# Kernel optimization log

Measured on AMD Instinct MI355X. Metric: run time of the kernel, lower is better.

The kernel has to match this reference:

```python
import jax, jax.numpy as jnp
import numpy as np

HEAD_DIM = 128
MROPE_SECTION = (16, 24, 24)  # sums to HEAD_DIM // 2
ROPE_THETA = 1000000.0
NEG_INF = -2.3819763e38


def _mrope_cos_sin(positions, theta, mrope_section, head_dim):
    # positions: [3, B, T] int; returns cos, sin of shape [B, T, head_dim]
    half = head_dim // 2
    inv_freq = 1.0 / (theta ** (jnp.arange(half, dtype=jnp.float32) * 2.0 / head_dim))
    angles = positions.astype(jnp.float32)[..., None] * inv_freq  # [3, B, T, half]
    sec = np.cumsum([0] + list(mrope_section))
    # pick temporal/height/width channel per frequency band
    angles_sel = jnp.concatenate(
        [angles[j, ..., sec[j]:sec[j + 1]] for j in range(3)], axis=-1
    )  # [B, T, half]
    cos = jnp.cos(angles_sel)
    sin = jnp.sin(angles_sel)
    cos = jnp.concatenate([cos, cos], axis=-1)  # [B, T, head_dim]
    sin = jnp.concatenate([sin, sin], axis=-1)
    return cos, sin


def _apply_rope(x, cos, sin):
    # x: [B, T, n, H]; cos/sin: [B, T, H]
    half = x.shape[-1] // 2
    x1, x2 = x[..., :half], x[..., half:]
    rot = jnp.concatenate([-x2, x1], axis=-1)
    return x * cos[:, :, None, :] + rot * sin[:, :, None, :]


def setup_inputs() -> dict:
    key = jax.random.key(0)
    ks = jax.random.split(key, 8)
    B, T, D = 2, 512, 3584
    N, K, H = 28, 4, 128
    S_CACHE = 3584
    S = S_CACHE + T
    x = jax.random.normal(ks[0], (B, T, D), dtype=jnp.float32)
    wq = jax.random.normal(ks[1], (N, D, H), dtype=jnp.float32) * (D ** -0.5)
    wk = jax.random.normal(ks[2], (K, D, H), dtype=jnp.float32) * (D ** -0.5)
    wv = jax.random.normal(ks[3], (K, D, H), dtype=jnp.float32) * (D ** -0.5)
    wo = jax.random.normal(ks[4], (N, H, D), dtype=jnp.float32) * ((N * H) ** -0.5)
    cache_k = jax.random.normal(ks[5], (B, S_CACHE, K, H), dtype=jnp.float32)
    cache_v = jax.random.normal(ks[6], (B, S_CACHE, K, H), dtype=jnp.float32)
    # positions continue after the cache; all 3 mrope channels identical (text)
    pos1d = S_CACHE + jnp.arange(T, dtype=jnp.int32)
    positions = jnp.broadcast_to(pos1d[None, None, :], (3, B, T))
    # mask: full visibility into cache, causal within the new block
    causal = jnp.tril(jnp.ones((T, T), dtype=bool))
    attn_mask = jnp.concatenate(
        [jnp.ones((T, S_CACHE), dtype=bool), causal], axis=-1
    )[None, None].repeat(B, axis=0)  # [B, 1, T, S]
    return {"x": x, "positions": positions, "attn_mask": attn_mask,
            "cache_k": cache_k, "cache_v": cache_v,
            "wq": wq, "wk": wk, "wv": wv, "wo": wo}


def reference(x, positions, attn_mask, cache_k, cache_v, wq, wk, wv, wo):
    N, K, H = wq.shape[0], wk.shape[0], wq.shape[2]
    G = N // K
    q = jnp.einsum('BTD,NDH->BTNH', x, wq)
    k = jnp.einsum('BSD,KDH->BSKH', x, wk)
    v = jnp.einsum('BSD,KDH->BSKH', x, wv)
    cos, sin = _mrope_cos_sin(positions, ROPE_THETA, MROPE_SECTION, H)
    q = _apply_rope(q, cos, sin)
    k = _apply_rope(k, cos, sin)
    q = q * (H ** -0.5)
    k = jnp.concatenate([cache_k, k], axis=1)  # [B, S, K, H]
    v = jnp.concatenate([cache_v, v], axis=1)
    cached_k, cached_v = k, v
    B, T = q.shape[0], q.shape[1]
    qg = q.reshape(B, T, K, G, H)
    # GQA: broadcast each kv head over its G query-head group (same math as repeat_kv)
    logits = jnp.einsum('BTKGH,BSKH->BKGTS', qg, k,
                        preferred_element_type=jnp.float32)
    masked = jnp.where(attn_mask[:, :, None, :, :], logits, NEG_INF)
    probs = jax.nn.softmax(masked, axis=-1).astype(x.dtype)
    encoded = jnp.einsum('BKGTS,BSKH->BTKGH', probs, v).reshape(B, T, N, H)
    out = jnp.einsum('BTNH,NHD->BTD', encoded, wo)
    return out, cached_k, cached_v
```

## Files before the change

kernel.cpp:

```cpp
#include <hip/hip_runtime.h>
#include <cstdint>
#include <cstddef>
#include <cmath>

typedef __bf16 bf16;
typedef __bf16 bf16x8 __attribute__((ext_vector_type(8)));
typedef float f32x4 __attribute__((ext_vector_type(4)));

__device__ __forceinline__ f32x4 mfma_bf16(bf16x8 a, bf16x8 b, f32x4 c) {
  return __builtin_amdgcn_mfma_f32_16x16x32_bf16(a, b, c, 0, 0, 0);
}

union U8 { bf16 h[8]; uint4 u; };
__device__ __forceinline__ uint4 cvt8(float4 a, float4 b) {
  U8 t;
  t.h[0] = (bf16)a.x; t.h[1] = (bf16)a.y; t.h[2] = (bf16)a.z; t.h[3] = (bf16)a.w;
  t.h[4] = (bf16)b.x; t.h[5] = (bf16)b.y; t.h[6] = (bf16)b.z; t.h[7] = (bf16)b.w;
  return t.u;
}

__device__ __forceinline__ bf16x8 ones8() {
  union { uint4 u; bf16x8 h; } t;
  t.u = make_uint4(0x3F803F80u, 0x3F803F80u, 0x3F803F80u, 0x3F803F80u);
  return t.h;
}

__device__ __forceinline__ void gload_lds16(const bf16* g, bf16* l) {
  __builtin_amdgcn_global_load_lds((const __attribute__((address_space(1))) void*)g,
                                   (__attribute__((address_space(3))) void*)l, 16, 0, 0);
}

__global__ __launch_bounds__(256) void prep(const float* __restrict__ ck,
                                            const float* __restrict__ cv,
                                            float* __restrict__ cko,
                                            float* __restrict__ cvo,
                                            bf16* __restrict__ kb_t,
                                            const float* __restrict__ x,
                                            bf16* __restrict__ xb,
                                            const int* __restrict__ pos,
                                            float* __restrict__ cosb,
                                            float* __restrict__ sinb) {
  size_t idx = (size_t)blockIdx.x * 256 + threadIdx.x;
  size_t e = idx * 8;
  size_t b = e / 1835008u, re = e % 1835008u;
  size_t de = b * 2097152u + re;
  float4 k0 = *(const float4*)(ck + e), k1 = *(const float4*)(ck + e + 4);
  float4 v0 = *(const float4*)(cv + e), v1 = *(const float4*)(cv + e + 4);
  *(float4*)(cko + de) = k0; *(float4*)(cko + de + 4) = k1;
  *(float4*)(cvo + de) = v0; *(float4*)(cvo + de + 4) = v1;
  {
    int s = (int)(re >> 9);
    int rem = (int)(re & 511);
    int khh = rem >> 7, h0 = rem & 127;
    size_t dk = ((size_t)(b * 4 + khh) * 128 + (s >> 5)) * 4096 + (size_t)(s & 31) * 128 + h0;
    *(uint4*)(kb_t + dk) = cvt8(k0, k1);
  }
  *(uint4*)(xb + e) = cvt8(*(const float4*)(x + e), *(const float4*)(x + e + 4));
  if (idx < 65536) {
    int m = (int)(idx >> 6), i = (int)(idx & 63);
    int j = (i < 16) ? 0 : ((i < 40) ? 1 : 2);
    float p = (float)pos[j * 1024 + m];
    float invf = (float)exp((double)i * -0.21586735246819178);
    float a = p * invf;
    cosb[m * 64 + i] = cosf(a);
    sinb[m * 64 + i] = sinf(a);
  }
}

__global__ __launch_bounds__(256) void transpose_f2b(const float* __restrict__ src,
                                                     bf16* __restrict__ dst,
                                                     int R, int C) {
  const size_t ms = (size_t)R * C;
  const float* s = src + (size_t)blockIdx.z * ms;
  bf16* d = dst + (size_t)blockIdx.z * ms;
  const int c0 = blockIdx.x * 64, r0 = blockIdx.y * 64;
  __shared__ bf16 tile[64 * 72];
  const int tid = threadIdx.x;
#pragma unroll
  for (int it = 0; it < 2; ++it) {
    int slot = tid + it * 256;
    int r = slot >> 3, c8 = slot & 7;
    const float* p = s + (size_t)(r0 + r) * C + c0 + c8 * 8;
    *(uint4*)(tile + r * 72 + c8 * 8) = cvt8(*(const float4*)p, *(const float4*)(p + 4));
  }
  __syncthreads();
#pragma unroll
  for (int it = 0; it < 2; ++it) {
    int slot = tid + it * 256;
    int c = slot >> 3, r8 = slot & 7;
    U8 tmp;
#pragma unroll
    for (int jj = 0; jj < 8; ++jj) tmp.h[jj] = tile[(r8 * 8 + jj) * 72 + c];
    *(uint4*)(d + (size_t)(c0 + c) * R + r0 + r8 * 8) = tmp.u;
  }
}

__global__ __launch_bounds__(256) void transpose_qkv(const float* __restrict__ wq,
                                                     const float* __restrict__ wk,
                                                     const float* __restrict__ wv,
                                                     bf16* __restrict__ dst) {
  const size_t ms = (size_t)3584 * 128;
  const int z = blockIdx.z;
  const float* s = (z < 28) ? wq + (size_t)z * ms
                 : (z < 32) ? wk + (size_t)(z - 28) * ms
                            : wv + (size_t)(z - 32) * ms;
  bf16* d = dst + (size_t)z * ms;
  const int c0 = blockIdx.x * 64, r0 = blockIdx.y * 64;
  __shared__ bf16 tile[64 * 72];
  const int tid = threadIdx.x;
#pragma unroll
  for (int it = 0; it < 2; ++it) {
    int slot = tid + it * 256;
    int r = slot >> 3, c8 = slot & 7;
    const float* p = s + (size_t)(r0 + r) * 128 + c0 + c8 * 8;
    *(uint4*)(tile + r * 72 + c8 * 8) = cvt8(*(const float4*)p, *(const float4*)(p + 4));
  }
  __syncthreads();
#pragma unroll
  for (int it = 0; it < 2; ++it) {
    int slot = tid + it * 256;
    int c = slot >> 3, r8 = slot & 7;
    U8 tmp;
#pragma unroll
    for (int jj = 0; jj < 8; ++jj) tmp.h[jj] = tile[(r8 * 8 + jj) * 72 + c];
    *(uint4*)(d + (size_t)(c0 + c) * 3584 + r0 + r8 * 8) = tmp.u;
  }
}

__global__ __launch_bounds__(256) void transpose_v(const float* __restrict__ cvo,
                                                   bf16* __restrict__ vt_t) {
  const int b = blockIdx.z >> 2, kh = blockIdx.z & 3;
  const int s0 = blockIdx.x * 64, h0 = blockIdx.y * 64;
  __shared__ bf16 tile[64 * 72];
  const int tid = threadIdx.x;
#pragma unroll
  for (int it = 0; it < 2; ++it) {
    int slot = tid + it * 256;
    int r = slot >> 3, c8 = slot & 7;
    const float* p = cvo + (size_t)((b * 4096 + s0 + r) * 4 + kh) * 128 + h0 + c8 * 8;
    *(uint4*)(tile + r * 72 + c8 * 8) = cvt8(*(const float4*)p, *(const float4*)(p + 4));
  }
  __syncthreads();
#pragma unroll
  for (int it = 0; it < 2; ++it) {
    int slot = tid + it * 256;
    int c = slot >> 3, r8 = slot & 7;
    U8 tmp;
#pragma unroll
    for (int jj = 0; jj < 8; ++jj) tmp.h[jj] = tile[(r8 * 8 + jj) * 72 + c];
    int s = s0 + r8 * 8;
    *(uint4*)(vt_t + ((size_t)((b * 4 + kh) * 128 + (s >> 5))) * 4096 +
              (size_t)(h0 + c) * 32 + (s & 31)) = tmp.u;
  }
}

template <int MODE>
__global__ __launch_bounds__(256) void gemm128(
    const bf16* __restrict__ A, const bf16* __restrict__ Bt,
    bf16* __restrict__ q_ws, float* __restrict__ cko, bf16* __restrict__ kb_t,
    float* __restrict__ cvo, const float* __restrict__ cosb,
    const float* __restrict__ sinb, float* __restrict__ outp) {
  const int cb = blockIdx.x;
  const int m0 = blockIdx.y * 128;
  const int tid = threadIdx.x;
  const int wave = tid >> 6, lane = tid & 63;
  const int c16 = lane & 15, q4 = lane >> 4;
  __shared__ bf16 lA[2][128 * 64];
  __shared__ bf16 lB[2][128 * 64];

  int offA[2][2], offB[8][2];
#pragma unroll
  for (int i = 0; i < 2; ++i) {
    int rA = wave * 32 + i * 16 + c16;
#pragma unroll
    for (int kk = 0; kk < 2; ++kk) offA[i][kk] = rA * 64 + (kk * 4 + q4) * 8;
  }
#pragma unroll
  for (int j = 0; j < 8; ++j) {
    int rB = j * 16 + c16;
#pragma unroll
    for (int kk = 0; kk < 2; ++kk) offB[j][kk] = rB * 64 + (kk * 4 + q4) * 8;
  }

  f32x4 acc[2][8];
#pragma unroll
  for (int i = 0; i < 2; ++i)
#pragma unroll
    for (int j = 0; j < 8; ++j) acc[i][j] = (f32x4){0.f, 0.f, 0.f, 0.f};

#pragma unroll
  for (int it = 0; it < 4; ++it) {
    int slot = tid + it * 256;
    gload_lds16(A + (size_t)(m0 + (slot >> 3)) * 3584 + (slot & 7) * 8, &lA[0][slot * 8]);
    gload_lds16(Bt + (size_t)(cb * 128 + (slot >> 3)) * 3584 + (slot & 7) * 8, &lB[0][slot * 8]);
  }
  __syncthreads();

  for (int k0 = 0; k0 < 3584; k0 += 64) {
    const int cur = (k0 >> 6) & 1;
    if (k0 + 64 < 3584) {
#pragma unroll
      for (int it = 0; it < 4; ++it) {
        int slot = tid + it * 256;
        gload_lds16(A + (size_t)(m0 + (slot >> 3)) * 3584 + k0 + 64 + (slot & 7) * 8,
                    &lA[cur ^ 1][slot * 8]);
        gload_lds16(Bt + (size_t)(cb * 128 + (slot >> 3)) * 3584 + k0 + 64 + (slot & 7) * 8,
                    &lB[cur ^ 1][slot * 8]);
      }
    }
#pragma unroll
    for (int kk = 0; kk < 2; ++kk) {
      bf16x8 av0 = *(const bf16x8*)(&lA[cur][offA[0][kk]]);
      bf16x8 av1 = *(const bf16x8*)(&lA[cur][offA[1][kk]]);
#pragma unroll
      for (int j = 0; j < 8; ++j) {
        bf16x8 bv = *(const bf16x8*)(&lB[cur][offB[j][kk]]);
        acc[0][j] = mfma_bf16(av0, bv, acc[0][j]);
        acc[1][j] = mfma_bf16(av1, bv, acc[1][j]);
      }
    }
    __syncthreads();
  }

  if (MODE == 1) {
#pragma unroll
    for (int i = 0; i < 2; ++i) {
      int mb = m0 + wave * 32 + i * 16 + q4 * 4;
#pragma unroll
      for (int r = 0; r < 4; ++r) {
        size_t rowoff = (size_t)(mb + r) * 3584 + cb * 128;
#pragma unroll
        for (int j = 0; j < 8; ++j) outp[rowoff + j * 16 + c16] = acc[i][j][r];
      }
    }
    return;
  }

  const int head = cb;
#pragma unroll
  for (int i = 0; i < 2; ++i) {
    int mb = m0 + wave * 32 + i * 16 + q4 * 4;
#pragma unroll
    for (int r = 0; r < 4; ++r) {
      int m = mb + r;
      int bb = m >> 9, tt = m & 511;
      if (head < 32) {
        const float* cp = cosb + m * 64;
        const float* sp = sinb + m * 64;
#pragma unroll
        for (int j = 0; j < 4; ++j) {
          int h = j * 16 + c16;
          float c = cp[h], s = sp[h];
          float v1 = acc[i][j][r], v2 = acc[i][j + 4][r];
          float o1 = v1 * c - v2 * s;
          float o2 = v2 * c + v1 * s;
          if (head < 28) {
            const float QS = 0.08838834764831845f;
            size_t base = ((size_t)m * 28 + head) * 128;
            q_ws[base + h] = (bf16)(o1 * QS);
            q_ws[base + h + 64] = (bf16)(o2 * QS);
          } else {
            int sg = 3584 + tt;
            size_t base = ((size_t)((bb * 4096 + sg) * 4 + (head - 28))) * 128;
            cko[base + h] = o1;
            cko[base + h + 64] = o2;
            size_t bt = ((size_t)(bb * 4 + (head - 28)) * 128 + (sg >> 5)) * 4096 +
                        (size_t)(sg & 31) * 128;
            kb_t[bt + h] = (bf16)o1;
            kb_t[bt + h + 64] = (bf16)o2;
          }
        }
      } else {
        size_t base = ((size_t)((bb * 4096 + 3584 + tt) * 4 + (head - 32))) * 128;
#pragma unroll
        for (int j = 0; j < 8; ++j) cvo[base + j * 16 + c16] = acc[i][j][r];
      }
    }
  }
}

__global__ __launch_bounds__(512) void attn_kernel(const bf16* __restrict__ q_ws,
                                                   const bf16* __restrict__ kb_t,
                                                   const bf16* __restrict__ vt_t,
                                                   bf16* __restrict__ p0,
                                                   bf16* __restrict__ p1,
                                                   bf16* __restrict__ p2,
                                                   float* __restrict__ lp) {
  const int combo = blockIdx.x & 7;
  const int b = combo >> 2, kh = combo & 3;
  const int rest = blockIdx.x >> 3;
  const int third = rest % 3;
  const int t0 = (rest / 3) * 16;
  const int tid = threadIdx.x;
  const int wave = tid >> 6, lane = tid & 63;
  const int c16 = lane & 15, q4 = lane >> 4;

  __shared__ bf16 Kc[2][4096];
  __shared__ bf16 Vc[2][4096];
  __shared__ bf16 Ps[8][16 * 40];

  const int kr = tid >> 4, ksl = tid & 15;
  const int ksrc = kr * 128 + ((ksl ^ (kr & 7)) * 8);
  const int vh = tid >> 2, vsl = tid & 3;
  const int vsrc = vh * 32 + ((vsl ^ ((vh >> 1) & 3)) * 8);
  const bf16* kcb = kb_t + (size_t)((b * 4 + kh) * 128) * 4096;
  const bf16* vcb = vt_t + (size_t)((b * 4 + kh) * 128) * 4096;

  int koff[2][4];
#pragma unroll
  for (int kk = 0; kk < 4; ++kk) {
    int ph = ((q4 * 16 + kk * 64) ^ ((c16 & 7) << 4)) >> 1;
    koff[0][kk] = c16 * 128 + ph;
    koff[1][kk] = (c16 + 16) * 128 + ph;
  }
  int voff[8];
#pragma unroll
  for (int jo = 0; jo < 8; ++jo)
    voff[jo] = (jo * 16 + c16) * 32 + ((q4 ^ ((c16 >> 1) & 3)) * 8);

  const int n = kh * 7 + wave;
  bf16x8 aQ[4];
  if (wave < 7) {
    const bf16* qbase = q_ws + ((size_t)((b * 512 + t0 + c16) * 28 + n)) * 128 + q4 * 8;
#pragma unroll
    for (int kk = 0; kk < 4; ++kk) aQ[kk] = *(const bf16x8*)(qbase + kk * 32);
  }

  f32x4 accO[8];
  f32x4 accL = (f32x4){0.f, 0.f, 0.f, 0.f};
#pragma unroll
  for (int j = 0; j < 8; ++j) accO[j] = (f32x4){0.f, 0.f, 0.f, 0.f};
  const bf16x8 vone = ones8();
  bf16* pw = Ps[wave];

  const int nch = (3631 + t0) >> 5;
  const int lo = (nch * third) / 3, hi = (nch * (third + 1)) / 3;

  gload_lds16(kcb + (size_t)lo * 4096 + ksrc, &Kc[0][tid * 8]);
  gload_lds16(vcb + (size_t)lo * 4096 + vsrc, &Vc[0][tid * 8]);
  __syncthreads();

  for (int c = lo; c < hi; ++c) {
    const int cur = (c - lo) & 1;
    if (c + 1 < hi) {
      gload_lds16(kcb + (size_t)(c + 1) * 4096 + ksrc, &Kc[cur ^ 1][tid * 8]);
      gload_lds16(vcb + (size_t)(c + 1) * 4096 + vsrc, &Vc[cur ^ 1][tid * 8]);
    }
    if (wave < 7) {
      const int s0 = c * 32;
      const bf16* kc = Kc[cur];
      const bf16* vc = Vc[cur];
      f32x4 accS0 = (f32x4){0.f, 0.f, 0.f, 0.f};
      f32x4 accS1 = (f32x4){0.f, 0.f, 0.f, 0.f};
#pragma unroll
      for (int kk = 0; kk < 4; ++kk) {
        bf16x8 bK0 = *(const bf16x8*)(&kc[koff[0][kk]]);
        bf16x8 bK1 = *(const bf16x8*)(&kc[koff[1][kk]]);
        accS0 = mfma_bf16(aQ[kk], bK0, accS0);
        accS1 = mfma_bf16(aQ[kk], bK1, accS1);
      }

      if (s0 + 31 > 3584 + t0) {
#pragma unroll
        for (int r = 0; r < 4; ++r) {
          int lim = 3584 + t0 + q4 * 4 + r - s0;
          float x0 = (c16 <= lim) ? __expf(accS0[r]) : 0.f;
          float x1 = (16 + c16 <= lim) ? __expf(accS1[r]) : 0.f;
          int prow = (q4 * 4 + r) * 40;
          pw[prow + c16] = (bf16)x0;
          pw[prow + 16 + c16] = (bf16)x1;
        }
      } else {
#pragma unroll
        for (int r = 0; r < 4; ++r) {
          int prow = (q4 * 4 + r) * 40;
          pw[prow + c16] = (bf16)__expf(accS0[r]);
          pw[prow + 16 + c16] = (bf16)__expf(accS1[r]);
        }
      }

      bf16x8 aP = *(const bf16x8*)(pw + c16 * 40 + q4 * 8);
      accL = mfma_bf16(aP, vone, accL);
#pragma unroll
      for (int jo = 0; jo < 8; ++jo) {
        bf16x8 bV = *(const bf16x8*)(&vc[voff[jo]]);
        accO[jo] = mfma_bf16(aP, bV, accO[jo]);
      }
    }
    __syncthreads();
  }

  if (wave < 7) {
    bf16* pb = (third == 0) ? p0 : (third == 1) ? p1 : p2;
#pragma unroll
    for (int r = 0; r < 4; ++r) {
      int tg = t0 + q4 * 4 + r;
      size_t row = (size_t)(b * 512 + tg) * 28 + n;
      size_t base = row * 128;
#pragma unroll
      for (int jo = 0; jo < 8; ++jo)
        pb[base + jo * 16 + c16] = (bf16)accO[jo][r];
      if (c16 == 0) lp[third * 57344 + row] = accL[r];
    }
  }
}

__global__ __launch_bounds__(256) void attn_merge(const bf16* __restrict__ p0,
                                                  const bf16* __restrict__ p1,
                                                  const bf16* __restrict__ p2,
                                                  const float* __restrict__ lp,
                                                  bf16* __restrict__ enc) {
  size_t idx = (size_t)blockIdx.x * 256 + threadIdx.x;
  size_t e = idx * 8;
  size_t row = e >> 7;
  float l = lp[row] + lp[57344 + row] + lp[114688 + row];
  float inv = 1.0f / l;
  bf16x8 a = *(const bf16x8*)(p0 + e);
  bf16x8 b8 = *(const bf16x8*)(p1 + e);
  bf16x8 c8 = *(const bf16x8*)(p2 + e);
  U8 o;
#pragma unroll
  for (int j = 0; j < 8; ++j)
    o.h[j] = (bf16)(((float)a[j] + (float)b8[j] + (float)c8[j]) * inv);
  *(uint4*)(enc + e) = o.u;
}

extern "C" void kernel_launch(void* const* d_in, const int* in_sizes, int n_in,
                              void* d_out, int out_size, void* d_ws, size_t ws_size,
                              hipStream_t stream) {
  const float* x = (const float*)d_in[0];
  const int* pos = (const int*)d_in[1];
  const float* ck = (const float*)d_in[3];
  const float* cv = (const float*)d_in[4];
  const float* wq = (const float*)d_in[5];
  const float* wk = (const float*)d_in[6];
  const float* wv = (const float*)d_in[7];
  const float* wo = (const float*)d_in[8];

  float* out = (float*)d_out;
  float* cko = out + 3670016;
  float* cvo = cko + 4194304;

  bf16* wqkvT = (bf16*)d_ws;
  bf16* woT = wqkvT;
  bf16* p2 = wqkvT + 12845056;
  bf16* xb = wqkvT + 16515072;
  bf16* q_ws = xb + 3670016;
  bf16* encw = q_ws + 3670016;
  bf16* kb_t = encw + 3670016;
  bf16* vt_t = kb_t + 4194304;
  float* cosb = (float*)(vt_t + 4194304);
  float* sinb = cosb + 65536;
  float* lp = out;
  if (ws_size < 72351744ull) return;

  prep<<<1792, 256, 0, stream>>>(ck, cv, cko, cvo, kb_t, x, xb, pos, cosb, sinb);
  transpose_qkv<<<dim3(2, 56, 36), 256, 0, stream>>>(wq, wk, wv, wqkvT);
  gemm128<0><<<dim3(36, 8), 256, 0, stream>>>(xb, wqkvT, q_ws, cko, kb_t, cvo, cosb, sinb, nullptr);
  transpose_f2b<<<dim3(56, 56, 1), 256, 0, stream>>>(wo, woT, 3584, 3584);
  transpose_v<<<dim3(64, 2, 8), 256, 0, stream>>>(cvo, vt_t);
  attn_kernel<<<768, 512, 0, stream>>>(q_ws, kb_t, vt_t, encw, xb, p2, lp);
  attn_merge<<<1792, 256, 0, stream>>>(encw, xb, p2, lp, encw);
  gemm128<1><<<dim3(28, 8), 256, 0, stream>>>(encw, woT, nullptr, nullptr, nullptr, nullptr,
                                              nullptr, nullptr, out);
}
```

Baseline: 471.9 us.

## Use 512-thread GEMM blocks and register-shuffle P in attention instead of LDS

The GEMM kernels now launch 512 threads per 128x128 tile, with each of 8 waves owning 16 rows instead of 32. This halves accumulators per thread and raises wave count per CU, which may help latency hiding. The attention kernel swaps the MFMA operand order so S is produced transposed, then packs exp(S) to bf16 in registers and redistributes it with shfl_xor and v_permlane32_swap. This removes the per-chunk LDS round trip for P and its scratch buffer, at the cost of extra cross-lane instructions and reliance on the correct lane mapping.

```diff
diff --git a/kernel.cpp b/kernel.cpp
--- a/kernel.cpp
+++ b/kernel.cpp
@@ -28,6 +28,12 @@
 __device__ __forceinline__ void gload_lds16(const bf16* g, bf16* l) {
   __builtin_amdgcn_global_load_lds((const __attribute__((address_space(1))) void*)g,
                                    (__attribute__((address_space(3))) void*)l, 16, 0, 0);
+}
+
+__device__ __forceinline__ unsigned cvt_pk_bf16(float lo, float hi) {
+  unsigned r;
+  asm("v_cvt_pk_bf16_f32 %0, %1, %2" : "=v"(r) : "v"(lo), "v"(hi));
+  return r;
 }
 
 __global__ __launch_bounds__(256) void prep(const float* __restrict__ ck,
@@ -155,7 +161,7 @@
 }
 
 template <int MODE>
-__global__ __launch_bounds__(256) void gemm128(
+__global__ __launch_bounds__(512) void gemm128(
     const bf16* __restrict__ A, const bf16* __restrict__ Bt,
     bf16* __restrict__ q_ws, float* __restrict__ cko, bf16* __restrict__ kb_t,
     float* __restrict__ cvo, const float* __restrict__ cosb,
@@ -168,13 +174,9 @@
   __shared__ bf16 lA[2][128 * 64];
   __shared__ bf16 lB[2][128 * 64];
 
-  int offA[2][2], offB[8][2];
-#pragma unroll
-  for (int i = 0; i < 2; ++i) {
-    int rA = wave * 32 + i * 16 + c16;
-#pragma unroll
-    for (int kk = 0; kk < 2; ++kk) offA[i][kk] = rA * 64 + (kk * 4 + q4) * 8;
-  }
+  int offA[2], offB[8][2];
+#pragma unroll
+  for (int kk = 0; kk < 2; ++kk) offA[kk] = (wave * 16 + c16) * 64 + (kk * 4 + q4) * 8;
 #pragma unroll
   for (int j = 0; j < 8; ++j) {
     int rB = j * 16 + c16;
@@ -182,15 +184,13 @@
     for (int kk = 0; kk < 2; ++kk) offB[j][kk] = rB * 64 + (kk * 4 + q4) * 8;
   }
 
-  f32x4 acc[2][8];
-#pragma unroll
-  for (int i = 0; i < 2; ++i)
-#pragma unroll
-    for (int j = 0; j < 8; ++j) acc[i][j] = (f32x4){0.f, 0.f, 0.f, 0.f};
-
-#pragma unroll
-  for (int it = 0; it < 4; ++it) {
-    int slot = tid + it * 256;
+  f32x4 acc[8];
+#pragma unroll
+  for (int j = 0; j < 8; ++j) acc[j] = (f32x4){0.f, 0.f, 0.f, 0.f};
+
+#pragma unroll
+  for (int it = 0; it < 2; ++it) {
+    int slot = tid + it * 512;
     gload_lds16(A + (size_t)(m0 + (slot >> 3)) * 3584 + (slot & 7) * 8, &lA[0][slot * 8]);
     gload_lds16(Bt + (size_t)(cb * 128 + (slot >> 3)) * 3584 + (slot & 7) * 8, &lB[0][slot * 8]);
   }
@@ -200,8 +200,8 @@
     const int cur = (k0 >> 6) & 1;
     if (k0 + 64 < 3584) {
 #pragma unroll
-      for (int it = 0; it < 4; ++it) {
-        int slot = tid + it * 256;
+      for (int it = 0; it < 2; ++it) {
+        int slot = tid + it * 512;
         gload_lds16(A + (size_t)(m0 + (slot >> 3)) * 3584 + k0 + 64 + (slot & 7) * 8,
                     &lA[cur ^ 1][slot * 8]);
         gload_lds16(Bt + (size_t)(cb * 128 + (slot >> 3)) * 3584 + k0 + 64 + (slot & 7) * 8,
@@ -210,71 +210,63 @@
     }
 #pragma unroll
     for (int kk = 0; kk < 2; ++kk) {
-      bf16x8 av0 = *(const bf16x8*)(&lA[cur][offA[0][kk]]);
-      bf16x8 av1 = *(const bf16x8*)(&lA[cur][offA[1][kk]]);
+      bf16x8 av = *(const bf16x8*)(&lA[cur][offA[kk]]);
 #pragma unroll
       for (int j = 0; j < 8; ++j) {
         bf16x8 bv = *(const bf16x8*)(&lB[cur][offB[j][kk]]);
-        acc[0][j] = mfma_bf16(av0, bv, acc[0][j]);
-        acc[1][j] = mfma_bf16(av1, bv, acc[1][j]);
+        acc[j] = mfma_bf16(av, bv, acc[j]);
       }
     }
     __syncthreads();
   }
 
   if (MODE == 1) {
-#pragma unroll
-    for (int i = 0; i < 2; ++i) {
-      int mb = m0 + wave * 32 + i * 16 + q4 * 4;
-#pragma unroll
-      for (int r = 0; r < 4; ++r) {
-        size_t rowoff = (size_t)(mb + r) * 3584 + cb * 128;
-#pragma unroll
-        for (int j = 0; j < 8; ++j) outp[rowoff + j * 16 + c16] = acc[i][j][r];
-      }
+    int mb = m0 + wave * 16 + q4 * 4;
+#pragma unroll
+    for (int r = 0; r < 4; ++r) {
+      size_t rowoff = (size_t)(mb + r) * 3584 + cb * 128;
+#pragma unroll
+      for (int j = 0; j < 8; ++j) outp[rowoff + j * 16 + c16] = acc[j][r];
     }
     return;
   }
 
   const int head = cb;
-#pragma unroll
-  for (int i = 0; i < 2; ++i) {
-    int mb = m0 + wave * 32 + i * 16 + q4 * 4;
-#pragma unroll
-    for (int r = 0; r < 4; ++r) {
-      int m = mb + r;
-      int bb = m >> 9, tt = m & 511;
-      if (head < 32) {
-        const float* cp = cosb + m * 64;
-        const float* sp = sinb + m * 64;
-#pragma unroll
-        for (int j = 0; j < 4; ++j) {
-          int h = j * 16 + c16;
-          float c = cp[h], s = sp[h];
-          float v1 = acc[i][j][r], v2 = acc[i][j + 4][r];
-          float o1 = v1 * c - v2 * s;
-          float o2 = v2 * c + v1 * s;
-          if (head < 28) {
-            const float QS = 0.08838834764831845f;
-            size_t base = ((size_t)m * 28 + head) * 128;
-            q_ws[base + h] = (bf16)(o1 * QS);
-            q_ws[base + h + 64] = (bf16)(o2 * QS);
-          } else {
-            int sg = 3584 + tt;
-            size_t base = ((size_t)((bb * 4096 + sg) * 4 + (head - 28))) * 128;
-            cko[base + h] = o1;
-            cko[base + h + 64] = o2;
-            size_t bt = ((size_t)(bb * 4 + (head - 28)) * 128 + (sg >> 5)) * 4096 +
-                        (size_t)(sg & 31) * 128;
-            kb_t[bt + h] = (bf16)o1;
-            kb_t[bt + h + 64] = (bf16)o2;
-          }
+  int mb = m0 + wave * 16 + q4 * 4;
+#pragma unroll
+  for (int r = 0; r < 4; ++r) {
+    int m = mb + r;
+    int bb = m >> 9, tt = m & 511;
+    if (head < 32) {
+      const float* cp = cosb + m * 64;
+      const float* sp = sinb + m * 64;
+#pragma unroll
+      for (int j = 0; j < 4; ++j) {
+        int h = j * 16 + c16;
+        float c = cp[h], s = sp[h];
+        float v1 = acc[j][r], v2 = acc[j + 4][r];
+        float o1 = v1 * c - v2 * s;
+        float o2 = v2 * c + v1 * s;
+        if (head < 28) {
+          const float QS = 0.08838834764831845f;
+          size_t base = ((size_t)m * 28 + head) * 128;
+          q_ws[base + h] = (bf16)(o1 * QS);
+          q_ws[base + h + 64] = (bf16)(o2 * QS);
+        } else {
+          int sg = 3584 + tt;
+          size_t base = ((size_t)((bb * 4096 + sg) * 4 + (head - 28))) * 128;
+          cko[base + h] = o1;
+          cko[base + h + 64] = o2;
+          size_t bt = ((size_t)(bb * 4 + (head - 28)) * 128 + (sg >> 5)) * 4096 +
+                      (size_t)(sg & 31) * 128;
+          kb_t[bt + h] = (bf16)o1;
+          kb_t[bt + h + 64] = (bf16)o2;
         }
-      } else {
-        size_t base = ((size_t)((bb * 4096 + 3584 + tt) * 4 + (head - 32))) * 128;
-#pragma unroll
-        for (int j = 0; j < 8; ++j) cvo[base + j * 16 + c16] = acc[i][j][r];
-      }
+      }
+    } else {
+      size_t base = ((size_t)((bb * 4096 + 3584 + tt) * 4 + (head - 32))) * 128;
+#pragma unroll
+      for (int j = 0; j < 8; ++j) cvo[base + j * 16 + c16] = acc[j][r];
     }
   }
 }
@@ -297,7 +289,6 @@
 
   __shared__ bf16 Kc[2][4096];
   __shared__ bf16 Vc[2][4096];
-  __shared__ bf16 Ps[8][16 * 40];
 
   const int kr = tid >> 4, ksl = tid & 15;
   const int ksrc = kr * 128 + ((ksl ^ (kr & 7)) * 8);
@@ -331,7 +322,7 @@
 #pragma unroll
   for (int j = 0; j < 8; ++j) accO[j] = (f32x4){0.f, 0.f, 0.f, 0.f};
   const bf16x8 vone = ones8();
-  bf16* pw = Ps[wave];
+  const bool odd = (q4 & 1) != 0;
 
   const int nch = (3631 + t0) >> 5;
   const int lo = (nch * third) / 3, hi = (nch * (third + 1)) / 3;
@@ -356,35 +347,63 @@
       for (int kk = 0; kk < 4; ++kk) {
         bf16x8 bK0 = *(const bf16x8*)(&kc[koff[0][kk]]);
         bf16x8 bK1 = *(const bf16x8*)(&kc[koff[1][kk]]);
-        accS0 = mfma_bf16(aQ[kk], bK0, accS0);
-        accS1 = mfma_bf16(aQ[kk], bK1, accS1);
-      }
-
+        accS0 = mfma_bf16(bK0, aQ[kk], accS0);
+        accS1 = mfma_bf16(bK1, aQ[kk], accS1);
+      }
+
+      float pv0[4], pv1[4];
       if (s0 + 31 > 3584 + t0) {
+        int lim = 3584 + t0 + c16 - s0;
 #pragma unroll
         for (int r = 0; r < 4; ++r) {
-          int lim = 3584 + t0 + q4 * 4 + r - s0;
-          float x0 = (c16 <= lim) ? __expf(accS0[r]) : 0.f;
-          float x1 = (16 + c16 <= lim) ? __expf(accS1[r]) : 0.f;
-          int prow = (q4 * 4 + r) * 40;
-          pw[prow + c16] = (bf16)x0;
-          pw[prow + 16 + c16] = (bf16)x1;
+          int sl = q4 * 4 + r;
+          pv0[r] = (sl <= lim) ? __expf(accS0[r]) : 0.f;
+          pv1[r] = (16 + sl <= lim) ? __expf(accS1[r]) : 0.f;
         }
       } else {
 #pragma unroll
         for (int r = 0; r < 4; ++r) {
-          int prow = (q4 * 4 + r) * 40;
-          pw[prow + c16] = (bf16)__expf(accS0[r]);
-          pw[prow + 16 + c16] = (bf16)__expf(accS1[r]);
+          pv0[r] = __expf(accS0[r]);
+          pv1[r] = __expf(accS1[r]);
         }
       }
 
-      bf16x8 aP = *(const bf16x8*)(pw + c16 * 40 + q4 * 8);
-      accL = mfma_bf16(aP, vone, accL);
+      unsigned u0 = cvt_pk_bf16(pv0[0], pv0[1]);
+      unsigned u1 = cvt_pk_bf16(pv0[2], pv0[3]);
+      unsigned u2 = cvt_pk_bf16(pv1[0], pv1[1]);
+      unsigned u3 = cvt_pk_bf16(pv1[2], pv1[3]);
+
+      unsigned x0 = (unsigned)__shfl_xor((int)u0, 16);
+      unsigned x1 = (unsigned)__shfl_xor((int)u1, 16);
+      unsigned x2 = (unsigned)__shfl_xor((int)u2, 16);
+      unsigned x3 = (unsigned)__shfl_xor((int)u3, 16);
+      unsigned Slo0 = odd ? x0 : u0, Slo1 = odd ? x1 : u1;
+      unsigned Slo2 = odd ? u0 : x0, Slo3 = odd ? u1 : x1;
+      unsigned Shi0 = odd ? x2 : u2, Shi1 = odd ? x3 : u3;
+      unsigned Shi2 = odd ? u2 : x2, Shi3 = odd ? u3 : x3;
+      unsigned f0, f1, f2, f3;
+      {
+        unsigned a = Slo0, bb2 = Shi0;
+        asm volatile("v_permlane32_swap_b32 %0, %1" : "+v"(a), "+v"(bb2));
+        f0 = odd ? bb2 : a;
+        a = Slo1; bb2 = Shi1;
+        asm volatile("v_permlane32_swap_b32 %0, %1" : "+v"(a), "+v"(bb2));
+        f1 = odd ? bb2 : a;
+        a = Slo2; bb2 = Shi2;
+        asm volatile("v_permlane32_swap_b32 %0, %1" : "+v"(a), "+v"(bb2));
+        f2 = odd ? bb2 : a;
+        a = Slo3; bb2 = Shi3;
+        asm volatile("v_permlane32_swap_b32 %0, %1" : "+v"(a), "+v"(bb2));
+        f3 = odd ? bb2 : a;
+      }
+      union { uint4 u; bf16x8 h; } ap;
+      ap.u = make_uint4(f0, f1, f2, f3);
+
+      accL = mfma_bf16(ap.h, vone, accL);
 #pragma unroll
       for (int jo = 0; jo < 8; ++jo) {
         bf16x8 bV = *(const bf16x8*)(&vc[voff[jo]]);
-        accO[jo] = mfma_bf16(aP, bV, accO[jo]);
+        accO[jo] = mfma_bf16(ap.h, bV, accO[jo]);
       }
     }
     __syncthreads();
@@ -456,11 +475,11 @@
 
   prep<<<1792, 256, 0, stream>>>(ck, cv, cko, cvo, kb_t, x, xb, pos, cosb, sinb);
   transpose_qkv<<<dim3(2, 56, 36), 256, 0, stream>>>(wq, wk, wv, wqkvT);
-  gemm128<0><<<dim3(36, 8), 256, 0, stream>>>(xb, wqkvT, q_ws, cko, kb_t, cvo, cosb, sinb, nullptr);
+  gemm128<0><<<dim3(36, 8), 512, 0, stream>>>(xb, wqkvT, q_ws, cko, kb_t, cvo, cosb, sinb, nullptr);
   transpose_f2b<<<dim3(56, 56, 1), 256, 0, stream>>>(wo, woT, 3584, 3584);
   transpose_v<<<dim3(64, 2, 8), 256, 0, stream>>>(cvo, vt_t);
   attn_kernel<<<768, 512, 0, stream>>>(q_ws, kb_t, vt_t, encw, xb, p2, lp);
   attn_merge<<<1792, 256, 0, stream>>>(encw, xb, p2, lp, encw);
-  gemm128<1><<<dim3(28, 8), 256, 0, stream>>>(encw, woT, nullptr, nullptr, nullptr, nullptr,
+  gemm128<1><<<dim3(28, 8), 512, 0, stream>>>(encw, woT, nullptr, nullptr, nullptr, nullptr,
                                               nullptr, nullptr, out);
 }
```

Result: slower. 531.1 us (+12.5%).
